# Kernel optimization log

Hardware: AMD Instinct MI355X
Metric: run time of the kernel (lower is better)

Reference implementation:

```python
import jax, jax.numpy as jnp
import numpy as np

# Module config (init_kwargs)
CIN, COUT, KH, KW = 256, 256, 3, 3
STRIDE, PADDING = 1, 1
T = 64                 # psum chunk size along the reduction (K) axis
NBITS = 8              # saturating accumulator bits (signed)
QMAX = (1 << (NBITS - 1)) - 1   # 127
QMIN = QMAX - (1 << NBITS) + 1  # -128


def setup_inputs() -> dict:
    key = jax.random.key(0)
    k1, k2 = jax.random.split(key)
    x = jax.random.normal(k1, (8, CIN, 56, 56), dtype=jnp.float32)
    # nn.Parameter(torch.rand((N,1)) * 0.001)
    weights = jax.random.uniform(k2, (CIN * COUT * KH * KW, 1), dtype=jnp.float32) * 0.001
    return {"x": x, "weights": weights}


def reference(x, weights):
    B, _, H, W = x.shape
    OH = (H - KH + 2 * PADDING) // STRIDE + 1
    OW = (W - KW + 2 * PADDING) // STRIDE + 1

    w = weights.reshape(COUT, CIN, KH, KW)
    # per-output-channel scaling factor, detached
    scale = jax.lax.stop_gradient(jnp.mean(jnp.abs(w), axis=(1, 2, 3), keepdims=True))
    # binarize with STE: sign(w).detach() - clamp(w).detach() + clamp(w)
    wc = jnp.clip(w, -1.0, 1.0)
    wb = jax.lax.stop_gradient(jnp.sign(w) - wc) + wc

    # unfold (im2col); channel varies slowest -> matches torch.nn.functional.unfold
    patches = jax.lax.conv_general_dilated_patches(
        x, (KH, KW), (STRIDE, STRIDE), [(PADDING, PADDING), (PADDING, PADDING)]
    )  # [B, CIN*KH*KW, OH*OW... (spatial)]
    K = CIN * KH * KW
    L = OH * OW
    A = patches.reshape(B, K, L).transpose(0, 2, 1)  # [B, L, K]
    X = wb.reshape(COUT, K).T                        # [K, COUT]

    pad = (-K) % T
    if pad:
        A = jnp.pad(A, ((0, 0), (0, 0), (0, pad)))
        X = jnp.pad(X, ((0, pad), (0, 0)))
    nT = (K + pad) // T

    A4 = A.reshape(B, L, nT, T)        # chunked reduction axis
    X3 = X.reshape(nT, T, COUT)
    # per-chunk partial sums (satmm_cuda.forward_psum)
    psum = jnp.einsum('blnt,ntc->nblc', A4, X3)  # [nT, B, L, COUT]

    # saturating sequential accumulation: reduce(lambda a,b: clip(a+b, QMIN, QMAX))
    def step(carry, p):
        return jnp.clip(carry + p, QMIN, QMAX), None
    y_flat, _ = jax.lax.scan(step, psum[0], psum[1:])  # [B, L, COUT]

    y = y_flat.transpose(0, 2, 1).reshape(B, COUT, OH, OW)
    y = y * scale.reshape(1, -1, 1, 1)
    # psum returned in the original [B, L, COUT, nT] layout
    return y, psum.transpose(1, 2, 3, 0)
```

## Files before the change

### kernel.cpp

```cpp
#include <hip/hip_runtime.h>
#include <hip/hip_bf16.h>

#define CIN 256
#define COUT 256
#define HW 56
#define BATCH 8
#define L_SPATIAL 3136
#define K_TOTAL 2304
#define NT 36
#define NH 18
#define ROWF (COUT * NT)
#define KSTRIDE 2312
#define ATILE_BYTES (16 * KSTRIDE * 2)
#define STAGE_OFF ATILE_BYTES
#define CARRY_OFF (ATILE_BYTES + 73728)
#define LDS_BYTES (CARRY_OFF + 8192)
#define MT_TOTAL 1568
#define TILES_PER_IMG 196
#define QMAXF 127.0f
#define QMINF -128.0f

typedef short bf16x8 __attribute__((ext_vector_type(8)));
typedef float f32x4 __attribute__((ext_vector_type(4)));
typedef float f32x2 __attribute__((ext_vector_type(2)));

__device__ __forceinline__ void nt_store4(float* p, f32x4 v) {
  __builtin_nontemporal_store(v, reinterpret_cast<f32x4*>(p));
}

__device__ __forceinline__ void lgkm_barrier() {
  __builtin_amdgcn_sched_barrier(0);
  asm volatile("s_waitcnt lgkmcnt(0)" ::: "memory");
  __builtin_amdgcn_s_barrier();
  asm volatile("" ::: "memory");
  __builtin_amdgcn_sched_barrier(0);
}

__global__ __launch_bounds__(256) void prep_kernel(
    const float* __restrict__ w, unsigned short* __restrict__ bsign,
    float* __restrict__ scale) {
  const int c = blockIdx.x;
  const int t = threadIdx.x;
  const float* row = w + (size_t)c * K_TOTAL;
  unsigned short* out = bsign + (size_t)c * K_TOTAL;
  float acc = 0.0f;
#pragma unroll
  for (int j = 0; j < 9; ++j) {
    const int k = t + 256 * j;
    const float v = row[k];
    acc += __builtin_fabsf(v);
    out[k] = (v > 0.0f) ? (unsigned short)0x3F80
           : ((v < 0.0f) ? (unsigned short)0xBF80 : (unsigned short)0);
  }
#pragma unroll
  for (int o = 32; o > 0; o >>= 1) acc += __shfl_down(acc, o, 64);
  __shared__ float red[4];
  if ((t & 63) == 0) red[t >> 6] = acc;
  __syncthreads();
  if (t == 0) scale[c] = (red[0] + red[1] + red[2] + red[3]) * (1.0f / 2304.0f);
}

template <int H>
__device__ __forceinline__ void compute18(
    const unsigned short* __restrict__ aptr,
    const unsigned short* __restrict__ bptr,
    f32x4* __restrict__ ps, f32x4& sacc) {
  const f32x4 zero = {0.0f, 0.0f, 0.0f, 0.0f};
  const unsigned short* ap = aptr + H * NH * 64;
  const unsigned short* bp = bptr + H * NH * 64;
  bf16x8 b0 = *reinterpret_cast<const bf16x8*>(bp);
  bf16x8 b1 = *reinterpret_cast<const bf16x8*>(bp + 32);
#pragma unroll
  for (int j = 0; j < NH; ++j) {
    bf16x8 nb0, nb1;
    if (j + 1 < NH) {
      nb0 = *reinterpret_cast<const bf16x8*>(bp + (j + 1) * 64);
      nb1 = *reinterpret_cast<const bf16x8*>(bp + (j + 1) * 64 + 32);
    }
    bf16x8 a0 = *reinterpret_cast<const bf16x8*>(ap + j * 64);
    bf16x8 a1 = *reinterpret_cast<const bf16x8*>(ap + j * 64 + 32);
    f32x4 acc = __builtin_amdgcn_mfma_f32_16x16x32_bf16(a0, b0, zero, 0, 0, 0);
    acc = __builtin_amdgcn_mfma_f32_16x16x32_bf16(a1, b1, acc, 0, 0, 0);
    ps[j] = acc;
    if (H == 0) {
      if (j == 0) {
        sacc = acc;
      } else {
#pragma unroll
        for (int e = 0; e < 4; ++e)
          sacc[e] = __builtin_amdgcn_fmed3f(sacc[e] + acc[e], QMINF, QMAXF);
      }
    }
    b0 = nb0;
    b1 = nb1;
  }
}

__global__ __launch_bounds__(1024, 4) void satconv_kernel(
    const float* __restrict__ x, const unsigned short* __restrict__ bsign,
    const float* __restrict__ scale, float* __restrict__ y_out,
    float* __restrict__ psum_out) {
  extern __shared__ char smem[];
  unsigned short* Atile = (unsigned short*)smem;
  float* stage = (float*)(smem + STAGE_OFF);
  float* carryb = (float*)(smem + CARRY_OFF);

  const int tid = threadIdx.x;
  const int bid = blockIdx.x;
  const int m_tile = (bid & 7) * TILES_PER_IMG + (bid >> 3);
  const int m0 = m_tile << 4;

  {
    const int ml = tid & 15;
    const int grp = tid >> 4;
    const int m = m0 + ml;
    const int b = m / L_SPATIAL;
    const int l = m - b * L_SPATIAL;
    const int oh = l / HW;
    const int ow = l - oh * HW;
    const float* xb = x + (size_t)b * (CIN * L_SPATIAL);
    unsigned short* arow = Atile + ml * KSTRIDE;
    for (int r = grp; r < 768; r += 64) {
      const int ci = r / 3;
      const int kh = r - ci * 3;
      const int hh = oh + kh - 1;
      const bool hv = ((unsigned)hh < (unsigned)HW);
      const float* xr = xb + (ci * HW + hh) * HW;
      const int kb = ci * 9 + kh * 3;
#pragma unroll
      for (int kw = 0; kw < 3; ++kw) {
        const int wv = ow + kw - 1;
        float v = 0.0f;
        if (hv && ((unsigned)wv < (unsigned)HW)) v = xr[wv];
        __hip_bfloat16 bv = __float2bfloat16(v);
        arow[kb + kw] = *reinterpret_cast<unsigned short*>(&bv);
      }
    }
  }

  const int lane = tid & 63;
  const int wave = tid >> 6;
  const int cl = lane & 15;
  const int q = lane >> 4;
  const int cs = wave >> 1;
  const int h = wave & 1;

  const float sc_s0 = scale[cs * 16 + cl];
  const float sc_s1 = scale[128 + cs * 16 + cl];

  int base_it[9];
  {
#pragma unroll
    for (int it = 0; it < 9; ++it) {
      const int f = it * 256 + lane * 4;
      const int qq = f / 576;
      const int rem = f - qq * 576;
      const int ci = rem / 36;
      const int n0 = rem - ci * 36;
      base_it[it] = ((m0 + (qq << 2)) * COUT + ci) * NT + n0;
    }
  }

  __syncthreads();

  const unsigned short* aptr = Atile + cl * KSTRIDE + q * 8;
  const int b_img = m0 / L_SPATIAL;
  const int l0 = m0 - b_img * L_SPATIAL;
  float* reg = stage + cs * 2304;

  for (int s = 0; s < 2; ++s) {
    const int csub0 = (s << 7) + (cs << 4);
    const int c = csub0 + cl;
    const unsigned short* bptr = bsign + (size_t)c * K_TOTAL + q * 8;

    f32x4 ps[NH];
    f32x4 sacc = {0.0f, 0.0f, 0.0f, 0.0f};
    if (h == 0) compute18<0>(aptr, bptr, ps, sacc);
    else        compute18<1>(aptr, bptr, ps, sacc);

    if (h == 0)
      *reinterpret_cast<f32x4*>(carryb + cs * 256 + lane * 4) = sacc;
    lgkm_barrier();
    if (h == 1) {
      f32x4 cin = *reinterpret_cast<const f32x4*>(carryb + cs * 256 + lane * 4);
#pragma unroll
      for (int j = 0; j < NH; ++j) {
#pragma unroll
        for (int e = 0; e < 4; ++e)
          cin[e] = __builtin_amdgcn_fmed3f(cin[e] + ps[j][e], QMINF, QMAXF);
      }
      const float sc = (s == 0) ? sc_s0 : sc_s1;
      f32x4 yv;
#pragma unroll
      for (int e = 0; e < 4; ++e) yv[e] = cin[e] * sc;
      nt_store4(y_out + ((size_t)b_img * COUT + c) * L_SPATIAL + l0 + (q << 2), yv);
    }

    const int soff = csub0 * NT;
#pragma unroll
    for (int rg = 0; rg < 4; ++rg) {
      {
        float* wr = reg + q * 576 + cl * 36 + h * NH;
        if (h == 0) {
          f32x4 v;
#pragma unroll
          for (int g = 0; g < 4; ++g) {
            v[0] = ps[4 * g + 0][rg]; v[1] = ps[4 * g + 1][rg];
            v[2] = ps[4 * g + 2][rg]; v[3] = ps[4 * g + 3][rg];
            *reinterpret_cast<f32x4*>(wr + 4 * g) = v;
          }
          f32x2 t = {ps[16][rg], ps[17][rg]};
          *reinterpret_cast<f32x2*>(wr + 16) = t;
        } else {
          f32x2 t = {ps[0][rg], ps[1][rg]};
          *reinterpret_cast<f32x2*>(wr) = t;
          f32x4 v;
#pragma unroll
          for (int g = 0; g < 4; ++g) {
            v[0] = ps[4 * g + 2][rg]; v[1] = ps[4 * g + 3][rg];
            v[2] = ps[4 * g + 4][rg]; v[3] = ps[4 * g + 5][rg];
            *reinterpret_cast<f32x4*>(wr + 2 + 4 * g) = v;
          }
        }
      }
      lgkm_barrier();
      {
        const int rgoff = rg * ROWF + soff;
        const int it0 = (h == 0) ? 0 : 5;
        const int it1 = (h == 0) ? 5 : 9;
        for (int it = it0; it < it1; ++it) {
          f32x4 v = *reinterpret_cast<const f32x4*>(reg + it * 256 + lane * 4);
          nt_store4(psum_out + (size_t)(base_it[it] + rgoff), v);
        }
      }
      lgkm_barrier();
    }
  }
}

extern "C" void kernel_launch(void* const* d_in, const int* in_sizes, int n_in,
                              void* d_out, int out_size, void* d_ws, size_t ws_size,
                              hipStream_t stream) {
  const float* x = (const float*)d_in[0];
  const float* w = (const float*)d_in[1];
  float* y = (float*)d_out;
  float* psum = y + (size_t)BATCH * COUT * L_SPATIAL;
  unsigned short* bsign = (unsigned short*)d_ws;
  float* scale = (float*)((char*)d_ws + (size_t)COUT * K_TOTAL * 2);

  prep_kernel<<<COUT, 256, 0, stream>>>(w, bsign, scale);

  hipFuncSetAttribute(reinterpret_cast<const void*>(satconv_kernel),
                      hipFuncAttributeMaxDynamicSharedMemorySize, LDS_BYTES);
  satconv_kernel<<<MT_TOTAL, 1024, LDS_BYTES, stream>>>(
      x, bsign, scale, y, psum);
}
```

Measured before the change: 1.194 ms.

## Make satconv kernel persistent with ping-pong LDS buffers for A tile and staging

Launches a fixed grid of 256 workgroups that loop over M tiles instead of one workgroup per tile. LDS becomes two buffers, alternating between im2col A tile and psum staging, so the next tile's A is built in the buffer the current tile just used for staging. B-operand prefetch deepens from one to two steps ahead. The aim is to cut launch overhead and reuse per-block setup, at the cost of more LDS per workgroup and an im2col build that still sits serially between tiles.

```diff
diff --git a/kernel.cpp b/kernel.cpp
--- a/kernel.cpp
+++ b/kernel.cpp
@@ -11,12 +11,12 @@
 #define NH 18
 #define ROWF (COUT * NT)
 #define KSTRIDE 2312
-#define ATILE_BYTES (16 * KSTRIDE * 2)
-#define STAGE_OFF ATILE_BYTES
-#define CARRY_OFF (ATILE_BYTES + 73728)
+#define BUF_BYTES (16 * KSTRIDE * 2)
+#define CARRY_OFF (2 * BUF_BYTES)
 #define LDS_BYTES (CARRY_OFF + 8192)
 #define MT_TOTAL 1568
 #define TILES_PER_IMG 196
+#define NWG 256
 #define QMAXF 127.0f
 #define QMINF -128.0f
 
@@ -60,6 +60,33 @@
   if (t == 0) scale[c] = (red[0] + red[1] + red[2] + red[3]) * (1.0f / 2304.0f);
 }
 
+__device__ __forceinline__ void build_atile(
+    const float* __restrict__ xb, unsigned short* __restrict__ Atile,
+    int tid, int l0) {
+  const int ml = tid & 15;
+  const int grp = tid >> 4;
+  const int l = l0 + ml;
+  const int oh = l / HW;
+  const int ow = l - oh * HW;
+  unsigned short* arow = Atile + ml * KSTRIDE;
+  for (int r = grp; r < 768; r += 64) {
+    const int ci = r / 3;
+    const int kh = r - ci * 3;
+    const int hh = oh + kh - 1;
+    const bool hv = ((unsigned)hh < (unsigned)HW);
+    const float* xr = xb + (ci * HW + hh) * HW;
+    const int kb = ci * 9 + kh * 3;
+#pragma unroll
+    for (int kw = 0; kw < 3; ++kw) {
+      const int wv = ow + kw - 1;
+      float v = 0.0f;
+      if (hv && ((unsigned)wv < (unsigned)HW)) v = xr[wv];
+      __hip_bfloat16 bv = __float2bfloat16(v);
+      arow[kb + kw] = *reinterpret_cast<unsigned short*>(&bv);
+    }
+  }
+}
+
 template <int H>
 __device__ __forceinline__ void compute18(
     const unsigned short* __restrict__ aptr,
@@ -68,19 +95,21 @@
   const f32x4 zero = {0.0f, 0.0f, 0.0f, 0.0f};
   const unsigned short* ap = aptr + H * NH * 64;
   const unsigned short* bp = bptr + H * NH * 64;
-  bf16x8 b0 = *reinterpret_cast<const bf16x8*>(bp);
-  bf16x8 b1 = *reinterpret_cast<const bf16x8*>(bp + 32);
+  bf16x8 b0[3], b1[3];
+  b0[0] = *reinterpret_cast<const bf16x8*>(bp);
+  b1[0] = *reinterpret_cast<const bf16x8*>(bp + 32);
+  b0[1] = *reinterpret_cast<const bf16x8*>(bp + 64);
+  b1[1] = *reinterpret_cast<const bf16x8*>(bp + 96);
 #pragma unroll
   for (int j = 0; j < NH; ++j) {
-    bf16x8 nb0, nb1;
-    if (j + 1 < NH) {
-      nb0 = *reinterpret_cast<const bf16x8*>(bp + (j + 1) * 64);
-      nb1 = *reinterpret_cast<const bf16x8*>(bp + (j + 1) * 64 + 32);
+    if (j + 2 < NH) {
+      b0[(j + 2) % 3] = *reinterpret_cast<const bf16x8*>(bp + (j + 2) * 64);
+      b1[(j + 2) % 3] = *reinterpret_cast<const bf16x8*>(bp + (j + 2) * 64 + 32);
     }
     bf16x8 a0 = *reinterpret_cast<const bf16x8*>(ap + j * 64);
     bf16x8 a1 = *reinterpret_cast<const bf16x8*>(ap + j * 64 + 32);
-    f32x4 acc = __builtin_amdgcn_mfma_f32_16x16x32_bf16(a0, b0, zero, 0, 0, 0);
-    acc = __builtin_amdgcn_mfma_f32_16x16x32_bf16(a1, b1, acc, 0, 0, 0);
+    f32x4 acc = __builtin_amdgcn_mfma_f32_16x16x32_bf16(a0, b0[j % 3], zero, 0, 0, 0);
+    acc = __builtin_amdgcn_mfma_f32_16x16x32_bf16(a1, b1[j % 3], acc, 0, 0, 0);
     ps[j] = acc;
     if (H == 0) {
       if (j == 0) {
@@ -91,8 +120,6 @@
           sacc[e] = __builtin_amdgcn_fmed3f(sacc[e] + acc[e], QMINF, QMAXF);
       }
     }
-    b0 = nb0;
-    b1 = nb1;
   }
 }
 
@@ -101,54 +128,24 @@
     const float* __restrict__ scale, float* __restrict__ y_out,
     float* __restrict__ psum_out) {
   extern __shared__ char smem[];
-  unsigned short* Atile = (unsigned short*)smem;
-  float* stage = (float*)(smem + STAGE_OFF);
   float* carryb = (float*)(smem + CARRY_OFF);
 
   const int tid = threadIdx.x;
-  const int bid = blockIdx.x;
-  const int m_tile = (bid & 7) * TILES_PER_IMG + (bid >> 3);
-  const int m0 = m_tile << 4;
-
-  {
-    const int ml = tid & 15;
-    const int grp = tid >> 4;
-    const int m = m0 + ml;
-    const int b = m / L_SPATIAL;
-    const int l = m - b * L_SPATIAL;
-    const int oh = l / HW;
-    const int ow = l - oh * HW;
-    const float* xb = x + (size_t)b * (CIN * L_SPATIAL);
-    unsigned short* arow = Atile + ml * KSTRIDE;
-    for (int r = grp; r < 768; r += 64) {
-      const int ci = r / 3;
-      const int kh = r - ci * 3;
-      const int hh = oh + kh - 1;
-      const bool hv = ((unsigned)hh < (unsigned)HW);
-      const float* xr = xb + (ci * HW + hh) * HW;
-      const int kb = ci * 9 + kh * 3;
-#pragma unroll
-      for (int kw = 0; kw < 3; ++kw) {
-        const int wv = ow + kw - 1;
-        float v = 0.0f;
-        if (hv && ((unsigned)wv < (unsigned)HW)) v = xr[wv];
-        __hip_bfloat16 bv = __float2bfloat16(v);
-        arow[kb + kw] = *reinterpret_cast<unsigned short*>(&bv);
-      }
-    }
-  }
+  const int w = blockIdx.x;
+  const int b_img = w & 7;
+  const float* xb = x + (size_t)b_img * (CIN * L_SPATIAL);
 
   const int lane = tid & 63;
-  const int wave = tid >> 6;
   const int cl = lane & 15;
   const int q = lane >> 4;
+  const int wave = tid >> 6;
   const int cs = wave >> 1;
   const int h = wave & 1;
 
   const float sc_s0 = scale[cs * 16 + cl];
   const float sc_s1 = scale[128 + cs * 16 + cl];
 
-  int base_it[9];
+  int rel_it[9];
   {
 #pragma unroll
     for (int it = 0; it < 9; ++it) {
@@ -157,84 +154,100 @@
       const int rem = f - qq * 576;
       const int ci = rem / 36;
       const int n0 = rem - ci * 36;
-      base_it[it] = ((m0 + (qq << 2)) * COUT + ci) * NT + n0;
-    }
-  }
-
+      rel_it[it] = ((qq << 2) * COUT + ci) * NT + n0;
+    }
+  }
+
+  int p = 0;
+  int t = w;
+  build_atile(xb, (unsigned short*)smem, tid, (t >> 3) << 4);
   __syncthreads();
 
-  const unsigned short* aptr = Atile + cl * KSTRIDE + q * 8;
-  const int b_img = m0 / L_SPATIAL;
-  const int l0 = m0 - b_img * L_SPATIAL;
-  float* reg = stage + cs * 2304;
-
-  for (int s = 0; s < 2; ++s) {
-    const int csub0 = (s << 7) + (cs << 4);
-    const int c = csub0 + cl;
-    const unsigned short* bptr = bsign + (size_t)c * K_TOTAL + q * 8;
-
-    f32x4 ps[NH];
-    f32x4 sacc = {0.0f, 0.0f, 0.0f, 0.0f};
-    if (h == 0) compute18<0>(aptr, bptr, ps, sacc);
-    else        compute18<1>(aptr, bptr, ps, sacc);
-
-    if (h == 0)
-      *reinterpret_cast<f32x4*>(carryb + cs * 256 + lane * 4) = sacc;
-    lgkm_barrier();
-    if (h == 1) {
-      f32x4 cin = *reinterpret_cast<const f32x4*>(carryb + cs * 256 + lane * 4);
-#pragma unroll
-      for (int j = 0; j < NH; ++j) {
-#pragma unroll
-        for (int e = 0; e < 4; ++e)
-          cin[e] = __builtin_amdgcn_fmed3f(cin[e] + ps[j][e], QMINF, QMAXF);
+  while (t < MT_TOTAL) {
+    const int l0 = (t >> 3) << 4;
+    const int m0 = (b_img * TILES_PER_IMG + (t >> 3)) << 4;
+    const int mbase = m0 * ROWF;
+    unsigned short* Atile = (unsigned short*)(smem + p * BUF_BYTES);
+    float* stage = (float*)(smem + (p ^ 1) * BUF_BYTES);
+    float* reg = stage + cs * 2304;
+    const unsigned short* aptr = Atile + cl * KSTRIDE + q * 8;
+
+    for (int s = 0; s < 2; ++s) {
+      const int csub0 = (s << 7) + (cs << 4);
+      const int c = csub0 + cl;
+      const unsigned short* bptr = bsign + (size_t)c * K_TOTAL + q * 8;
+
+      f32x4 ps[NH];
+      f32x4 sacc = {0.0f, 0.0f, 0.0f, 0.0f};
+      if (h == 0) compute18<0>(aptr, bptr, ps, sacc);
+      else        compute18<1>(aptr, bptr, ps, sacc);
+
+      if (h == 0)
+        *reinterpret_cast<f32x4*>(carryb + cs * 256 + lane * 4) = sacc;
+      lgkm_barrier();
+      if (h == 1) {
+        f32x4 cin = *reinterpret_cast<const f32x4*>(carryb + cs * 256 + lane * 4);
+#pragma unroll
+        for (int j = 0; j < NH; ++j) {
+#pragma unroll
+          for (int e = 0; e < 4; ++e)
+            cin[e] = __builtin_amdgcn_fmed3f(cin[e] + ps[j][e], QMINF, QMAXF);
+        }
+        const float sc = (s == 0) ? sc_s0 : sc_s1;
+        f32x4 yv;
+#pragma unroll
+        for (int e = 0; e < 4; ++e) yv[e] = cin[e] * sc;
+        nt_store4(y_out + ((size_t)b_img * COUT + c) * L_SPATIAL + l0 + (q << 2), yv);
       }
-      const float sc = (s == 0) ? sc_s0 : sc_s1;
-      f32x4 yv;
-#pragma unroll
-      for (int e = 0; e < 4; ++e) yv[e] = cin[e] * sc;
-      nt_store4(y_out + ((size_t)b_img * COUT + c) * L_SPATIAL + l0 + (q << 2), yv);
-    }
-
-    const int soff = csub0 * NT;
-#pragma unroll
-    for (int rg = 0; rg < 4; ++rg) {
-      {
-        float* wr = reg + q * 576 + cl * 36 + h * NH;
-        if (h == 0) {
-          f32x4 v;
-#pragma unroll
-          for (int g = 0; g < 4; ++g) {
-            v[0] = ps[4 * g + 0][rg]; v[1] = ps[4 * g + 1][rg];
-            v[2] = ps[4 * g + 2][rg]; v[3] = ps[4 * g + 3][rg];
-            *reinterpret_cast<f32x4*>(wr + 4 * g) = v;
-          }
-          f32x2 t = {ps[16][rg], ps[17][rg]};
-          *reinterpret_cast<f32x2*>(wr + 16) = t;
-        } else {
-          f32x2 t = {ps[0][rg], ps[1][rg]};
-          *reinterpret_cast<f32x2*>(wr) = t;
-          f32x4 v;
-#pragma unroll
-          for (int g = 0; g < 4; ++g) {
-            v[0] = ps[4 * g + 2][rg]; v[1] = ps[4 * g + 3][rg];
-            v[2] = ps[4 * g + 4][rg]; v[3] = ps[4 * g + 5][rg];
-            *reinterpret_cast<f32x4*>(wr + 2 + 4 * g) = v;
+
+      const int soff = csub0 * NT;
+#pragma unroll
+      for (int rg = 0; rg < 4; ++rg) {
+        {
+          float* wr = reg + q * 576 + cl * 36 + h * NH;
+          if (h == 0) {
+            f32x4 v;
+#pragma unroll
+            for (int g = 0; g < 4; ++g) {
+              v[0] = ps[4 * g + 0][rg]; v[1] = ps[4 * g + 1][rg];
+              v[2] = ps[4 * g + 2][rg]; v[3] = ps[4 * g + 3][rg];
+              *reinterpret_cast<f32x4*>(wr + 4 * g) = v;
+            }
+            f32x2 tl = {ps[16][rg], ps[17][rg]};
+            *reinterpret_cast<f32x2*>(wr + 16) = tl;
+          } else {
+            f32x2 tl = {ps[0][rg], ps[1][rg]};
+            *reinterpret_cast<f32x2*>(wr) = tl;
+            f32x4 v;
+#pragma unroll
+            for (int g = 0; g < 4; ++g) {
+              v[0] = ps[4 * g + 2][rg]; v[1] = ps[4 * g + 3][rg];
+              v[2] = ps[4 * g + 4][rg]; v[3] = ps[4 * g + 5][rg];
+              *reinterpret_cast<f32x4*>(wr + 2 + 4 * g) = v;
+            }
           }
         }
+        lgkm_barrier();
+        {
+          const int rgoff = rg * ROWF + soff;
+          const int it0 = (h == 0) ? 0 : 5;
+          const int it1 = (h == 0) ? 5 : 9;
+          for (int it = it0; it < it1; ++it) {
+            f32x4 v = *reinterpret_cast<const f32x4*>(reg + it * 256 + lane * 4);
+            nt_store4(psum_out + (size_t)(mbase + rel_it[it] + rgoff), v);
+          }
+        }
+        lgkm_barrier();
       }
-      lgkm_barrier();
-      {
-        const int rgoff = rg * ROWF + soff;
-        const int it0 = (h == 0) ? 0 : 5;
-        const int it1 = (h == 0) ? 5 : 9;
-        for (int it = it0; it < it1; ++it) {
-          f32x4 v = *reinterpret_cast<const f32x4*>(reg + it * 256 + lane * 4);
-          nt_store4(psum_out + (size_t)(base_it[it] + rgoff), v);
-        }
-      }
-      lgkm_barrier();
-    }
+    }
+
+    const int tn = t + NWG;
+    if (tn < MT_TOTAL)
+      build_atile(xb, (unsigned short*)(smem + (p ^ 1) * BUF_BYTES), tid,
+                  (tn >> 3) << 4);
+    lgkm_barrier();
+    p ^= 1;
+    t = tn;
   }
 }
 
@@ -252,6 +265,6 @@
 
   hipFuncSetAttribute(reinterpret_cast<const void*>(satconv_kernel),
                       hipFuncAttributeMaxDynamicSharedMemorySize, LDS_BYTES);
-  satconv_kernel<<<MT_TOTAL, 1024, LDS_BYTES, stream>>>(
+  satconv_kernel<<<NWG, 1024, LDS_BYTES, stream>>>(
       x, bsign, scale, y, psum);
 }
```

New measurement: 1.229 ms. 2.9% more time.
